# Optimization experiments

Hardware: AMD Instinct MI355X
Metric: run time of the kernel (lower is better)

## Reference

```python
import jax, jax.numpy as jnp
import numpy as np

N = 50000      # nodes
E = 400000     # edges
D = 128        # embedding_depth
H = 4          # attention heads
DK = 32        # per-head dim (graph_message_depth / heads)
NR = 50        # num_radial
L = 2          # num_graph_convolutions
NG = 100       # graphs in batch
NT = 100       # atom type vocab
TE = 32        # atom_type_embedding_dims
OUT = 512      # bottleneck_dim
CUT = 6.0      # convolution_cutoff


def setup_inputs() -> dict:
    key = jax.random.key(0)
    ks = jax.random.split(key, 20)
    s = 0.05
    inp = {
        'pos': jax.random.normal(ks[0], (N, 3), jnp.float32) * 5.0,
        'atom_types': jax.random.randint(ks[1], (N,), 0, NT),
        'edge_index': jax.random.randint(ks[2], (2, E), 0, N),
        'batch': jnp.sort(jax.random.randint(ks[3], (N,), 0, NG)),
        'emb_table': jax.random.normal(ks[4], (NT, TE), jnp.float32) * s,
        'W_init': jax.random.normal(ks[5], (TE + 3, D), jnp.float32) * s,
        'b_init': jnp.zeros((D,), jnp.float32),
        'Wq': jax.random.normal(ks[6], (L, D, H * DK), jnp.float32) * s,
        'Wk': jax.random.normal(ks[7], (L, D, H * DK), jnp.float32) * s,
        'Wv': jax.random.normal(ks[8], (L, D, H * DK), jnp.float32) * s,
        'We': jax.random.normal(ks[9], (L, NR, H * DK), jnp.float32) * s,
        'Wo': jax.random.normal(ks[10], (L, H * DK, D), jnp.float32) * s,
        'Wm1': jax.random.normal(ks[11], (L, D, D), jnp.float32) * s,
        'bm1': jnp.zeros((L, D), jnp.float32),
        'Wm2': jax.random.normal(ks[12], (L, D, D), jnp.float32) * s,
        'bm2': jnp.zeros((L, D), jnp.float32),
        'ln_g': jnp.ones((L, D), jnp.float32),
        'ln_b': jnp.zeros((L, D), jnp.float32),
        'W_out': jax.random.normal(ks[13], (D, OUT), jnp.float32) * s,
        'b_out': jnp.zeros((OUT,), jnp.float32),
    }
    return inp


def _layernorm(x, g, b):
    m = jnp.mean(x, -1, keepdims=True)
    v = jnp.var(x, -1, keepdims=True)
    return (x - m) * jax.lax.rsqrt(v + 1e-5) * g + b


def _rbf(d):
    # Gaussian radial basis with smooth cosine cutoff envelope
    mus = jnp.linspace(0.0, CUT, NR)
    gamma = (NR / CUT) ** 2
    env = 0.5 * (jnp.cos(jnp.pi * jnp.minimum(d, CUT) / CUT) + 1.0)
    return jnp.exp(-gamma * (d[:, None] - mus[None, :]) ** 2) * env[:, None]


def _seg_softmax(logits, seg, n):
    # logits: [E, H], segmented softmax over incoming edges per node
    m = jax.ops.segment_max(logits, seg, num_segments=n)
    e = jnp.exp(logits - m[seg])
    s = jax.ops.segment_sum(e, seg, num_segments=n)
    return e / (s[seg] + 1e-9)


def _forward(pos, atom_types, edge_index, batch, emb_table, W_init, b_init,
             Wq, Wk, Wv, We, Wo, Wm1, bm1, Wm2, bm2, ln_g, ln_b, W_out, b_out):
    src, dst = edge_index[0], edge_index[1]
    # atom type embedding + concat positions -> init node features
    x0 = jnp.concatenate([emb_table[atom_types], pos], axis=-1)  # [N, TE+3]
    x = x0 @ W_init + b_init                                     # [N, D]
    # radial features per edge
    d = jnp.linalg.norm(pos[src] - pos[dst] + 1e-8, axis=-1)     # [E]
    rb = _rbf(d)                                                 # [E, NR]
    scale = 1.0 / jnp.sqrt(jnp.float32(DK))
    for l in range(L):
        qn, kn, vn = x @ Wq[l], x @ Wk[l], x @ Wv[l]             # [N, H*DK]
        q = qn[dst].reshape(E, H, DK)
        k = kn[src].reshape(E, H, DK)
        v = vn[src].reshape(E, H, DK)
        e = (rb @ We[l]).reshape(E, H, DK)
        logits = jnp.sum(q * (k + e), axis=-1) * scale           # [E, H]
        a = _seg_softmax(logits, dst, N)                         # [E, H]
        msg = jax.ops.segment_sum(a[..., None] * (v + e), dst, num_segments=N)
        x = x + msg.reshape(N, H * DK) @ Wo[l]
        # nodewise FC block with pre-norm and residual
        h = _layernorm(x, ln_g[l], ln_b[l])
        h = jax.nn.gelu(h @ Wm1[l] + bm1[l])
        x = x + h @ Wm2[l] + bm2[l]
    # sum graph aggregation, then output projection to bottleneck
    g = jax.ops.segment_sum(x, batch, num_segments=NG)           # [NG, D]
    return g @ W_out + b_out                                     # [NG, OUT]


def reference(pos, atom_types, edge_index, batch, emb_table, W_init, b_init,
              Wq, Wk, Wv, We, Wo, Wm1, bm1, Wm2, bm2, ln_g, ln_b, W_out, b_out):
    return _forward(pos, atom_types, edge_index, batch, emb_table, W_init, b_init,
                    Wq, Wk, Wv, We, Wo, Wm1, bm1, Wm2, bm2, ln_g, ln_b, W_out, b_out)
```

## Files before the change

### kernel.cpp

```cpp
#include <hip/hip_runtime.h>
#include <math.h>

#define NN 50000
#define NE 400000
#define DDIM 128
#define NHEAD 4
#define NRAD 50
#define NGRAPH 100
#define NTYPE 100
#define TEMB 32
#define DOUT 512
#define CUTF 6.0f
#define PI_F 3.14159265358979323846f

#define SCAN_N ((NN + 255) / 256)

typedef unsigned int uint;
typedef unsigned short ushort;
typedef __attribute__((ext_vector_type(8))) short short8;
typedef __attribute__((ext_vector_type(4))) float f32x4;


__device__ __forceinline__ float gelu_tanh(float v) {
  float u = 0.7978845608028654f * (v + 0.044715f * v * v * v);
  return 0.5f * v * (1.0f + tanhf(u));
}

__device__ __forceinline__ ushort f2bf(float f) {
  uint u = __float_as_uint(f);
  uint r = (u + 0x7fffu + ((u >> 16) & 1u)) >> 16;
  return (ushort)r;
}
__device__ __forceinline__ float bfl(uint u) { return __uint_as_float(u << 16); }
__device__ __forceinline__ float bfh(uint u) { return __uint_as_float(u & 0xffff0000u); }

__device__ __forceinline__ float red16(float v) {
  v += __int_as_float(__builtin_amdgcn_update_dpp(0, __float_as_int(v), 0xB1, 0xF, 0xF, true));
  v += __int_as_float(__builtin_amdgcn_update_dpp(0, __float_as_int(v), 0x4E, 0xF, 0xF, true));
  v += __int_as_float(__builtin_amdgcn_update_dpp(0, __float_as_int(v), 0x141, 0xF, 0xF, true));
  v += __int_as_float(__builtin_amdgcn_update_dpp(0, __float_as_int(v), 0x140, 0xF, 0xF, true));
  return v;
}
__device__ __forceinline__ float red8(float v) {
  v += __int_as_float(__builtin_amdgcn_update_dpp(0, __float_as_int(v), 0xB1, 0xF, 0xF, true));
  v += __int_as_float(__builtin_amdgcn_update_dpp(0, __float_as_int(v), 0x4E, 0xF, 0xF, true));
  v += __int_as_float(__builtin_amdgcn_update_dpp(0, __float_as_int(v), 0x141, 0xF, 0xF, true));
  return v;
}

__global__ void k_fill_f(float* p, float v, int n) {
  int i = blockIdx.x * blockDim.x + threadIdx.x;
  if (i < n) p[i] = v;
}
__global__ void k_fill_i(int* p, int v, int n) {
  int i = blockIdx.x * blockDim.x + threadIdx.x;
  if (i < n) p[i] = v;
}


__global__ void k_wconv(const float* __restrict__ Wq, const float* __restrict__ Wk,
                        const float* __restrict__ Wv, const float* __restrict__ Wo,
                        const float* __restrict__ Wm1, const float* __restrict__ Wm2,
                        ushort* __restrict__ Wtb) {
  int idx = blockIdx.x * 256 + threadIdx.x;
  int m = idx >> 14;
  int r = idx & 16383;
  int c = r >> 7, k = r & 127;
  int l = m / 6, fam = m % 6;
  const float* src = fam == 0 ? Wq : fam == 1 ? Wk : fam == 2 ? Wv
                   : fam == 3 ? Wo : fam == 4 ? Wm1 : Wm2;
  Wtb[idx] = f2bf(src[l * 16384 + k * 128 + c]);
}


__global__ void k_wewo(const float* __restrict__ We, const float* __restrict__ Wo,
                       ushort* __restrict__ WW) {
  int idx = blockIdx.x * 256 + threadIdx.x;
  int l = idx >> 15;
  int r = idx & 32767;
  int c = r >> 8, k = r & 255;
  float acc = 0.f;
  if (k < 200) {
    int j = k >> 2, h = k & 3;
    const float* we = We + (size_t)l * NRAD * DDIM + j * DDIM + 32 * h;
    const float* wo = Wo + (size_t)l * DDIM * DDIM + (size_t)(32 * h) * DDIM + c;
#pragma unroll 8
    for (int dk = 0; dk < 32; ++dk) acc = fmaf(we[dk], wo[(size_t)dk * DDIM], acc);
  }
  WW[idx] = f2bf(acc);
}


__global__ void k_embw(const float* __restrict__ emb, const float* __restrict__ W,
                       const float* __restrict__ b, float* __restrict__ embW) {
  int idx = blockIdx.x * 256 + threadIdx.x;
  if (idx >= NTYPE * DDIM) return;
  int a = idx >> 7, c = idx & 127;
  const float* er = emb + (size_t)a * TEMB;
  float acc = b[c];
#pragma unroll
  for (int t = 0; t < TEMB; ++t) acc = fmaf(er[t], W[t * DDIM + c], acc);
  embW[idx] = acc;
}


__global__ void k_init2(const float* __restrict__ pos, const int* __restrict__ at,
                        const float* __restrict__ embW, const float* __restrict__ W,
                        float* __restrict__ x) {
  int idx = blockIdx.x * blockDim.x + threadIdx.x;
  if (idx >= NN * 32) return;
  int n = idx >> 5, c4 = (idx & 31) << 2;
  float4 e = *(const float4*)&embW[(size_t)at[n] * DDIM + c4];
  float px = pos[n * 3 + 0], py = pos[n * 3 + 1], pz = pos[n * 3 + 2];
  float4 wx = *(const float4*)&W[(TEMB + 0) * DDIM + c4];
  float4 wy = *(const float4*)&W[(TEMB + 1) * DDIM + c4];
  float4 wz = *(const float4*)&W[(TEMB + 2) * DDIM + c4];
  float4 o;
  o.x = e.x + px * wx.x + py * wy.x + pz * wz.x;
  o.y = e.y + px * wx.y + py * wy.y + pz * wz.y;
  o.z = e.z + px * wx.z + py * wy.z + pz * wz.z;
  o.w = e.w + px * wx.w + py * wy.w + pz * wz.w;
  *(float4*)&x[(size_t)n * DDIM + c4] = o;
}


__global__ void k_edge(const float* __restrict__ pos, const int* __restrict__ ei,
                       float* __restrict__ de, int* __restrict__ deg) {
  int e = blockIdx.x * blockDim.x + threadIdx.x;
  if (e >= NE) return;
  int s = ei[e], t = ei[NE + e];
  float dx = pos[s * 3 + 0] - pos[t * 3 + 0] + 1e-8f;
  float dy = pos[s * 3 + 1] - pos[t * 3 + 1] + 1e-8f;
  float dz = pos[s * 3 + 2] - pos[t * 3 + 2] + 1e-8f;
  de[e] = sqrtf(dx * dx + dy * dy + dz * dz);
  atomicAdd(&deg[t], 1);
}


__global__ void k_scan1(const int* __restrict__ deg, int* __restrict__ bsum) {
  __shared__ int red[256];
  int i = blockIdx.x * 256 + threadIdx.x;
  red[threadIdx.x] = (i < NN) ? deg[i] : 0;
  __syncthreads();
  for (int off = 128; off > 0; off >>= 1) {
    if (threadIdx.x < off) red[threadIdx.x] += red[threadIdx.x + off];
    __syncthreads();
  }
  if (threadIdx.x == 0) bsum[blockIdx.x] = red[0];
}

__global__ void k_scan2(int* __restrict__ bsum) {
  __shared__ int sh[256];
  int t = threadIdx.x;
  int v = (t < SCAN_N) ? bsum[t] : 0;
  sh[t] = v;
  __syncthreads();
  for (int off = 1; off < 256; off <<= 1) {
    int u = (t >= off) ? sh[t - off] : 0;
    __syncthreads();
    sh[t] += u;
    __syncthreads();
  }
  if (t < SCAN_N) bsum[t] = (t == 0) ? 0 : sh[t - 1];
}

__global__ void k_scan3(const int* __restrict__ deg, const int* __restrict__ bsum,
                        int* __restrict__ rowptr, int* __restrict__ cnear,
                        int* __restrict__ cfar) {
  __shared__ int sh[256];
  int t = threadIdx.x;
  int i = blockIdx.x * 256 + t;
  int v = (i < NN) ? deg[i] : 0;
  sh[t] = v;
  __syncthreads();
  for (int off = 1; off < 256; off <<= 1) {
    int u = (t >= off) ? sh[t - off] : 0;
    __syncthreads();
    sh[t] += u;
    __syncthreads();
  }
  int excl = bsum[blockIdx.x] + sh[t] - v;
  if (i < NN) {
    rowptr[i] = excl;
    cnear[i] = excl;
    cfar[i] = excl + v;
    if (i == NN - 1) rowptr[NN] = excl + v;
  }
}

__global__ void k_scatter(const int* __restrict__ ei, const float* __restrict__ de,
                          int* __restrict__ cnear, int* __restrict__ cfar,
                          int2* __restrict__ er) {
  int e = blockIdx.x * blockDim.x + threadIdx.x;
  if (e >= NE) return;
  int src = ei[e], dst = ei[NE + e];
  float d = de[e];
  int idx;
  if (d < CUTF)
    idx = atomicAdd(&cnear[dst], 1);
  else
    idx = atomicSub(&cfar[dst], 1) - 1;
  er[idx] = make_int2(src, __float_as_int(d));
}


__global__ __launch_bounds__(256) void k_qkv(
    const float* __restrict__ x, const ushort* __restrict__ Wt3,
    ushort* __restrict__ qo, ushort* __restrict__ ko, ushort* __restrict__ vo) {
  __shared__ ushort Al[128 * 128];
  __shared__ ushort Wl[128 * 128];
  const int tid = threadIdx.x;
  const int r0 = blockIdx.x * 128;

  for (int i = tid; i < 128 * 16; i += 256) {
    int r = i >> 4, g = i & 15;
    int gr = r0 + r;
    float4 f0 = {0, 0, 0, 0}, f1 = {0, 0, 0, 0};
    if (gr < NN) {
      f0 = *(const float4*)&x[(size_t)gr * 128 + g * 8];
      f1 = *(const float4*)&x[(size_t)gr * 128 + g * 8 + 4];
    }
    int gs = g ^ (r & 7);
    ushort4 u0 = {f2bf(f0.x), f2bf(f0.y), f2bf(f0.z), f2bf(f0.w)};
    ushort4 u1 = {f2bf(f1.x), f2bf(f1.y), f2bf(f1.z), f2bf(f1.w)};
    *(ushort4*)&Al[r * 128 + gs * 8] = u0;
    *(ushort4*)&Al[r * 128 + gs * 8 + 4] = u1;
  }

  const int w = tid >> 6, l = tid & 63;
  const int lg = l >> 4, lr = l & 15;

  for (int m = 0; m < 3; ++m) {
    for (int i = tid; i < 128 * 16; i += 256) {
      int c = i >> 4, g = i & 15;
      ushort4 w0 = *(const ushort4*)&Wt3[m * 16384 + c * 128 + g * 8];
      ushort4 w1 = *(const ushort4*)&Wt3[m * 16384 + c * 128 + g * 8 + 4];
      int gs = g ^ (c & 7);
      *(ushort4*)&Wl[c * 128 + gs * 8] = w0;
      *(ushort4*)&Wl[c * 128 + gs * 8 + 4] = w1;
    }
    __syncthreads();

    f32x4 acc[2][8];
#pragma unroll
    for (int rt = 0; rt < 2; ++rt)
#pragma unroll
      for (int ct = 0; ct < 8; ++ct) acc[rt][ct] = (f32x4){0.f, 0.f, 0.f, 0.f};

#pragma unroll
    for (int ks = 0; ks < 4; ++ks) {
      short8 af[2];
#pragma unroll
      for (int rt = 0; rt < 2; ++rt) {
        int arow = w * 32 + rt * 16 + lr;
        int ga = (ks * 4 + lg) ^ (arow & 7);
        af[rt] = *(const short8*)&Al[arow * 128 + ga * 8];
      }
#pragma unroll
      for (int ct = 0; ct < 8; ++ct) {
        int col = ct * 16 + lr;
        int gb = (ks * 4 + lg) ^ (col & 7);
        short8 bf = *(const short8*)&Wl[col * 128 + gb * 8];
#pragma unroll
        for (int rt = 0; rt < 2; ++rt)
          acc[rt][ct] = __builtin_amdgcn_mfma_f32_16x16x32_bf16(af[rt], bf, acc[rt][ct], 0, 0, 0);
      }
    }

    ushort* o = (m == 0) ? qo : (m == 1) ? ko : vo;
#pragma unroll
    for (int rt = 0; rt < 2; ++rt)
#pragma unroll
      for (int ct = 0; ct < 8; ++ct) {
        int col = ct * 16 + lr;
#pragma unroll
        for (int r = 0; r < 4; ++r) {
          int row = r0 + w * 32 + rt * 16 + lg * 4 + r;
          if (row < NN) o[(size_t)row * 128 + col] = f2bf(acc[rt][ct][r]);
        }
      }
    __syncthreads();
  }
}


template <bool BIAS, bool GELU, bool RESID, bool LNF, bool EXTK>
__global__ __launch_bounds__(256) void k_gemm2(
    const ushort* __restrict__ A, const ushort* __restrict__ Wt,
    const float* __restrict__ bias, const float* __restrict__ resid,
    void* __restrict__ outp, const float* __restrict__ lng,
    const float* __restrict__ lnb, ushort* __restrict__ lnout,
    const ushort* __restrict__ arbn, const ushort* __restrict__ WW) {
  __shared__ ushort Al[128 * 128];
  __shared__ ushort Wl[128 * 128];
  const int tid = threadIdx.x;
  const int r0 = blockIdx.x * 128;

  for (int i = tid; i < 128 * 16; i += 256) {
    int r = i >> 4, g = i & 15;
    int gr = r0 + r;
    ushort4 v0 = {0, 0, 0, 0}, v1 = {0, 0, 0, 0};
    if (gr < NN) {
      v0 = *(const ushort4*)&A[(size_t)gr * 128 + g * 8];
      v1 = *(const ushort4*)&A[(size_t)gr * 128 + g * 8 + 4];
    }
    int gs = g ^ (r & 7);
    *(ushort4*)&Al[r * 128 + gs * 8] = v0;
    *(ushort4*)&Al[r * 128 + gs * 8 + 4] = v1;
  }
  for (int i = tid; i < 128 * 16; i += 256) {
    int c = i >> 4, g = i & 15;
    ushort4 w0 = *(const ushort4*)&Wt[c * 128 + g * 8];
    ushort4 w1 = *(const ushort4*)&Wt[c * 128 + g * 8 + 4];
    int gs = g ^ (c & 7);
    *(ushort4*)&Wl[c * 128 + gs * 8] = w0;
    *(ushort4*)&Wl[c * 128 + gs * 8 + 4] = w1;
  }
  __syncthreads();

  const int w = tid >> 6, l = tid & 63;
  const int lg = l >> 4, lr = l & 15;
  f32x4 acc[2][8];
#pragma unroll
  for (int rt = 0; rt < 2; ++rt)
#pragma unroll
    for (int ct = 0; ct < 8; ++ct) acc[rt][ct] = (f32x4){0.f, 0.f, 0.f, 0.f};

#pragma unroll
  for (int ks = 0; ks < 4; ++ks) {
    short8 af[2];
#pragma unroll
    for (int rt = 0; rt < 2; ++rt) {
      int arow = w * 32 + rt * 16 + lr;
      int ga = (ks * 4 + lg) ^ (arow & 7);
      af[rt] = *(const short8*)&Al[arow * 128 + ga * 8];
    }
#pragma unroll
    for (int ct = 0; ct < 8; ++ct) {
      int col = ct * 16 + lr;
      int gb = (ks * 4 + lg) ^ (col & 7);
      short8 bf = *(const short8*)&Wl[col * 128 + gb * 8];
#pragma unroll
      for (int rt = 0; rt < 2; ++rt)
        acc[rt][ct] = __builtin_amdgcn_mfma_f32_16x16x32_bf16(af[rt], bf, acc[rt][ct], 0, 0, 0);
    }
  }

  if (EXTK) {
    for (int q = 0; q < 2; ++q) {
      __syncthreads();
      for (int i = tid; i < 128 * 16; i += 256) {
        int r = i >> 4, g = i & 15;
        int gr = r0 + r;
        ushort4 v0 = {0, 0, 0, 0}, v1 = {0, 0, 0, 0};
        if (gr < NN && (q == 0 || g < 9)) {
          v0 = *(const ushort4*)&arbn[(size_t)gr * 200 + q * 128 + g * 8];
          v1 = *(const ushort4*)&arbn[(size_t)gr * 200 + q * 128 + g * 8 + 4];
        }
        int gs = g ^ (r & 7);
        *(ushort4*)&Al[r * 128 + gs * 8] = v0;
        *(ushort4*)&Al[r * 128 + gs * 8 + 4] = v1;
      }
      for (int i = tid; i < 128 * 16; i += 256) {
        int c = i >> 4, g = i & 15;
        ushort4 w0 = *(const ushort4*)&WW[c * 256 + q * 128 + g * 8];
        ushort4 w1 = *(const ushort4*)&WW[c * 256 + q * 128 + g * 8 + 4];
        int gs = g ^ (c & 7);
        *(ushort4*)&Wl[c * 128 + gs * 8] = w0;
        *(ushort4*)&Wl[c * 128 + gs * 8 + 4] = w1;
      }
      __syncthreads();
#pragma unroll
      for (int ks = 0; ks < 4; ++ks) {
        short8 af[2];
#pragma unroll
        for (int rt = 0; rt < 2; ++rt) {
          int arow = w * 32 + rt * 16 + lr;
          int ga = (ks * 4 + lg) ^ (arow & 7);
          af[rt] = *(const short8*)&Al[arow * 128 + ga * 8];
        }
#pragma unroll
        for (int ct = 0; ct < 8; ++ct) {
          int col = ct * 16 + lr;
          int gb = (ks * 4 + lg) ^ (col & 7);
          short8 bf = *(const short8*)&Wl[col * 128 + gb * 8];
#pragma unroll
          for (int rt = 0; rt < 2; ++rt)
            acc[rt][ct] = __builtin_amdgcn_mfma_f32_16x16x32_bf16(af[rt], bf, acc[rt][ct], 0, 0, 0);
        }
      }
    }
  }

#pragma unroll
  for (int rt = 0; rt < 2; ++rt)
#pragma unroll
    for (int r = 0; r < 4; ++r) {
      int row = r0 + w * 32 + rt * 16 + lg * 4 + r;
      bool ok = row < NN;
      float v[8];
#pragma unroll
      for (int ct = 0; ct < 8; ++ct) {
        int col = ct * 16 + lr;
        float vv = acc[rt][ct][r];
        if (BIAS) vv += bias[col];
        if (GELU) vv = gelu_tanh(vv);
        if (RESID) vv += ok ? resid[(size_t)row * 128 + col] : 0.f;
        v[ct] = vv;
      }
      if (RESID || LNF) {
        if (ok)
#pragma unroll
          for (int ct = 0; ct < 8; ++ct)
            ((float*)outp)[(size_t)row * 128 + ct * 16 + lr] = v[ct];
      } else {
        if (ok)
#pragma unroll
          for (int ct = 0; ct < 8; ++ct)
            ((ushort*)outp)[(size_t)row * 128 + ct * 16 + lr] = f2bf(v[ct]);
      }
      if (LNF) {
        float s = 0.f, ss = 0.f;
#pragma unroll
        for (int ct = 0; ct < 8; ++ct) {
          s += v[ct];
          ss = fmaf(v[ct], v[ct], ss);
        }
#pragma unroll
        for (int msk = 8; msk >= 1; msk >>= 1) {
          s += __shfl_xor(s, msk);
          ss += __shfl_xor(ss, msk);
        }
        float mean = s * (1.0f / DDIM);
        float var = ss * (1.0f / DDIM) - mean * mean;
        float inv = rsqrtf(var + 1e-5f);
        if (ok)
#pragma unroll
          for (int ct = 0; ct < 8; ++ct) {
            int col = ct * 16 + lr;
            lnout[(size_t)row * 128 + col] =
                f2bf((v[ct] - mean) * inv * lng[col] + lnb[col]);
          }
      }
    }
}


__global__ __launch_bounds__(256) void k_qe(const ushort* __restrict__ qnb,
                                            const float* __restrict__ We,
                                            ushort* __restrict__ qe) {
  __shared__ float Wlds[NRAD][DDIM + 1];
  __shared__ float qlds[4][DDIM];
  int tid = threadIdx.x;
  for (int i = tid; i < NRAD * DDIM; i += 256) Wlds[i / DDIM][i % DDIM] = We[i];
  __syncthreads();
  int w = tid >> 6, t = tid & 63;
  for (int rep = 0; rep < 2; ++rep) {
    int n = blockIdx.x * 8 + rep * 4 + w;
    uint qu = *(const uint*)&qnb[(size_t)n * DDIM + 2 * t];
    qlds[w][2 * t] = bfl(qu);
    qlds[w][2 * t + 1] = bfh(qu);
    if (t < NRAD) {
      float e0 = 0.f, e1 = 0.f, e2 = 0.f, e3 = 0.f;
#pragma unroll
      for (int d = 0; d < 32; ++d) e0 = fmaf(Wlds[t][d], qlds[w][d], e0);
#pragma unroll
      for (int d = 32; d < 64; ++d) e1 = fmaf(Wlds[t][d], qlds[w][d], e1);
#pragma unroll
      for (int d = 64; d < 96; ++d) e2 = fmaf(Wlds[t][d], qlds[w][d], e2);
#pragma unroll
      for (int d = 96; d < 128; ++d) e3 = fmaf(Wlds[t][d], qlds[w][d], e3);
      ushort4 o = {f2bf(e0), f2bf(e1), f2bf(e2), f2bf(e3)};
      *(ushort4*)&qe[(size_t)n * 200 + 4 * t] = o;
    }
  }
}


__device__ __forceinline__ float rbf_fill(float d, int j) {
  const float step = CUTF / (NRAD - 1);
  const float gamma = (NRAD / CUTF) * (NRAD / CUTF);
  float mu = j * step;
  float dm = d - mu;
  float env = 0.5f * (__cosf(PI_F * d / CUTF) + 1.0f);
  return __expf(-gamma * dm * dm) * env;
}

#define SCALE_QK 0.17677669529663687f

__global__ __launch_bounds__(256) void k_attn7(
    const ushort* __restrict__ qnb, const ushort* __restrict__ knb,
    const ushort* __restrict__ vnb, ushort* __restrict__ qe,
    const int2* __restrict__ er, const int* __restrict__ rowptr,
    const int* __restrict__ nearend, ushort* __restrict__ msgb) {
  __shared__ float qel[4][64][4];
  __shared__ float rbl[4][64];
  __shared__ float aml[4][128];
  const int tid = threadIdx.x;

  const int w = tid >> 6, t = tid & 63;
  const int n = blockIdx.x * 4 + w;
  const int h = t >> 4;
  const int j0 = t & 15;
  const int hw = t >> 5;
  const int c = t & 31;
  uint qu = *(const uint*)&qnb[(size_t)n * DDIM + 2 * t];
  const float q0 = bfl(qu), q1 = bfh(qu);
  uint2 qp = *(const uint2*)&qnb[(size_t)n * DDIM + 4 * c];
  const float fq0 = bfl(qp.x), fq1 = bfh(qp.x), fq2 = bfl(qp.y), fq3 = bfh(qp.y);
  if (t < NRAD) {
    ushort4 qv = *(const ushort4*)&qe[(size_t)n * 200 + 4 * t];
    qel[w][t][0] = bfl(qv.x);
    qel[w][t][1] = bfl(qv.y);
    qel[w][t][2] = bfl(qv.z);
    qel[w][t][3] = bfl(qv.w);
  } else {
    qel[w][t][0] = 0.f; qel[w][t][1] = 0.f; qel[w][t][2] = 0.f; qel[w][t][3] = 0.f;
  }
  const int start = rowptr[n], nend = nearend[n], end = rowptr[n + 1];

  float s = 0.f, a0 = 0.f, a1 = 0.f;
  float4 arb = {0.f, 0.f, 0.f, 0.f};

  for (int cb = start; cb < nend; cb += 64) {
    int cnt = min(nend - cb, 64);
    int2 e_t = make_int2(0, 0);
    if (t < cnt) e_t = er[cb + t];
    for (int i = 0; i < cnt; ++i) {
      int src = __shfl(e_t.x, i);
      float dd = __shfl(__int_as_float(e_t.y), i);
      uint ku = *(const uint*)&knb[(size_t)src * DDIM + 2 * t];
      uint vu = *(const uint*)&vnb[(size_t)src * DDIM + 2 * t];
      float pr = q0 * bfl(ku) + q1 * bfh(ku);
      float rb = (t < NRAD) ? rbf_fill(dd, t) : 0.f;
      rbl[w][t] = rb;
      pr = fmaf(rbl[w][j0], qel[w][j0][h], pr);
      pr = fmaf(rbl[w][j0 + 16], qel[w][j0 + 16][h], pr);
      pr = fmaf(rbl[w][j0 + 32], qel[w][j0 + 32][h], pr);
      pr = fmaf(rbl[w][j0 + 48], qel[w][j0 + 48][h], pr);
      pr = red16(pr);
      float ae = __expf(fminf(pr * SCALE_QK, 60.f));
      s += ae;
      a0 = fmaf(ae, bfl(vu), a0);
      a1 = fmaf(ae, bfh(vu), a1);
      float aex = __shfl(ae, 0);
      float aey = __shfl(ae, 16);
      float aez = __shfl(ae, 32);
      float aew = __shfl(ae, 48);
      arb.x = fmaf(rb, aex, arb.x);
      arb.y = fmaf(rb, aey, arb.y);
      arb.z = fmaf(rb, aez, arb.z);
      arb.w = fmaf(rb, aew, arb.w);
    }
  }

  float sf = 0.f, af0 = 0.f, af1 = 0.f, af2 = 0.f, af3 = 0.f;
  for (int cb = nend; cb < end; cb += 64) {
    int cnt = min(end - cb, 64);
    int src_t = 0;
    if (t < cnt) src_t = er[cb + t].x;
    for (int i = hw; i < cnt; i += 2) {
      int src = __shfl(src_t, i);
      uint2 ku = *(const uint2*)&knb[(size_t)src * DDIM + 4 * c];
      uint2 vu = *(const uint2*)&vnb[(size_t)src * DDIM + 4 * c];
      float pr = fq0 * bfl(ku.x) + fq1 * bfh(ku.x);
      pr = fmaf(fq2, bfl(ku.y), pr);
      pr = fmaf(fq3, bfh(ku.y), pr);
      pr = red8(pr);
      float ae = __expf(fminf(pr * SCALE_QK, 60.f));
      sf += ae;
      af0 = fmaf(ae, bfl(vu.x), af0);
      af1 = fmaf(ae, bfh(vu.x), af1);
      af2 = fmaf(ae, bfl(vu.y), af2);
      af3 = fmaf(ae, bfh(vu.y), af3);
    }
  }
  sf += __shfl_xor(sf, 32);
  af0 += __shfl_xor(af0, 32);
  af1 += __shfl_xor(af1, 32);
  af2 += __shfl_xor(af2, 32);
  af3 += __shfl_xor(af3, 32);
  aml[w][4 * c + 0] = af0;
  aml[w][4 * c + 1] = af1;
  aml[w][4 * c + 2] = af2;
  aml[w][4 * c + 3] = af3;
  a0 += aml[w][2 * t];
  a1 += aml[w][2 * t + 1];

  float4 s4;
  s4.x = __shfl(s, 0) + __shfl(sf, 0);
  s4.y = __shfl(s, 16) + __shfl(sf, 8);
  s4.z = __shfl(s, 32) + __shfl(sf, 16);
  s4.w = __shfl(s, 48) + __shfl(sf, 24);
  float4 inv4 = {1.f / (s4.x + 1e-9f), 1.f / (s4.y + 1e-9f),
                 1.f / (s4.z + 1e-9f), 1.f / (s4.w + 1e-9f)};
  float invo = (h == 0) ? inv4.x : (h == 1) ? inv4.y : (h == 2) ? inv4.z : inv4.w;
  if (t < NRAD) {
    ushort4 o = {f2bf(arb.x * inv4.x), f2bf(arb.y * inv4.y),
                 f2bf(arb.z * inv4.z), f2bf(arb.w * inv4.w)};
    *(ushort4*)&qe[(size_t)n * 200 + 4 * t] = o;
  }
  a0 *= invo;
  a1 *= invo;
  uint pk = (uint)f2bf(a0) | ((uint)f2bf(a1) << 16);
  *(uint*)&msgb[(size_t)n * DDIM + 2 * t] = pk;
}


#define GS_NODES 32
__global__ void k_graphsum(const float* __restrict__ x, const int* __restrict__ batch,
                           float* __restrict__ g) {
  int t = threadIdx.x;
  int n0 = blockIdx.x * GS_NODES;
  int nend = n0 + GS_NODES;
  if (nend > NN) nend = NN;
  if (n0 >= NN) return;
  float acc = 0.f;
  int cur = batch[n0];
  for (int n = n0; n < nend; ++n) {
    int bb = batch[n];
    if (bb != cur) {
      atomicAdd(&g[(size_t)cur * DDIM + t], acc);
      acc = 0.f;
      cur = bb;
    }
    acc += x[(size_t)n * DDIM + t];
  }
  atomicAdd(&g[(size_t)cur * DDIM + t], acc);
}


__global__ void k_out(const float* __restrict__ g, const float* __restrict__ W,
                      const float* __restrict__ b, float* __restrict__ out) {
  int idx = blockIdx.x * blockDim.x + threadIdx.x;
  if (idx >= NGRAPH * DOUT) return;
  int r = idx / DOUT, c = idx % DOUT;
  float acc = b[c];
#pragma unroll 8
  for (int k = 0; k < DDIM; ++k) acc = fmaf(g[r * DDIM + k], W[k * DOUT + c], acc);
  out[idx] = acc;
}


extern "C" void kernel_launch(void* const* d_in, const int* in_sizes, int n_in,
                              void* d_out, int out_size, void* d_ws, size_t ws_size,
                              hipStream_t stream) {
  const float* pos = (const float*)d_in[0];
  const int* at = (const int*)d_in[1];
  const int* ei = (const int*)d_in[2];
  const int* batch = (const int*)d_in[3];
  const float* emb = (const float*)d_in[4];
  const float* W_init = (const float*)d_in[5];
  const float* b_init = (const float*)d_in[6];
  const float* Wq = (const float*)d_in[7];
  const float* Wk = (const float*)d_in[8];
  const float* Wv = (const float*)d_in[9];
  const float* We = (const float*)d_in[10];
  const float* Wo = (const float*)d_in[11];
  const float* Wm1 = (const float*)d_in[12];
  const float* bm1 = (const float*)d_in[13];
  const float* Wm2 = (const float*)d_in[14];
  const float* bm2 = (const float*)d_in[15];
  const float* ln_g = (const float*)d_in[16];
  const float* ln_b = (const float*)d_in[17];
  const float* W_out = (const float*)d_in[18];
  const float* b_out = (const float*)d_in[19];
  float* out = (float*)d_out;

  const size_t ND = (size_t)NN * DDIM;
  float* x = (float*)d_ws;
  ushort* qnb = (ushort*)(x + ND);
  ushort* knb = qnb + ND;
  ushort* vnb = knb + ND;
  ushort* msgb = vnb + ND;
  ushort* qe = msgb + ND;
  ushort* Wtb = qe + (size_t)NN * 200;
  ushort* WW = Wtb + 12 * 16384;
  float* embW = (float*)(WW + 2 * 32768);
  float* de = embW + NTYPE * DDIM;
  int* deg = (int*)(de + NE);
  int* cnear = deg + NN;
  int* cfar = cnear + NN;
  int* rowptr = cfar + NN;
  int2* er = (int2*)(rowptr + NN + 64);
  float* gb = (float*)(er + NE);
  int* bsum = (int*)(gb + NGRAPH * DDIM);

  ushort* hb = qnb;
  ushort* h2 = knb;

  k_wconv<<<12 * 16384 / 256, 256, 0, stream>>>(Wq, Wk, Wv, Wo, Wm1, Wm2, Wtb);
  k_wewo<<<2 * 32768 / 256, 256, 0, stream>>>(We, Wo, WW);
  k_embw<<<(NTYPE * DDIM + 255) / 256, 256, 0, stream>>>(emb, W_init, b_init, embW);
  k_fill_i<<<(NN + 255) / 256, 256, 0, stream>>>(deg, 0, NN);
  k_init2<<<(NN * 32 + 255) / 256, 256, 0, stream>>>(pos, at, embW, W_init, x);
  k_edge<<<(NE + 255) / 256, 256, 0, stream>>>(pos, ei, de, deg);
  k_scan1<<<SCAN_N, 256, 0, stream>>>(deg, bsum);
  k_scan2<<<1, 256, 0, stream>>>(bsum);
  k_scan3<<<SCAN_N, 256, 0, stream>>>(deg, bsum, rowptr, cnear, cfar);
  k_scatter<<<(NE + 255) / 256, 256, 0, stream>>>(ei, de, cnear, cfar, er);

  const int gg = (NN + 127) / 128;
  for (int l = 0; l < 2; ++l) {
    const ushort* Wt_l = Wtb + (size_t)l * 6 * 16384;
    const float* We_l = We + (size_t)l * NRAD * DDIM;
    const ushort* WW_l = WW + (size_t)l * 32768;

    k_qkv<<<gg, 256, 0, stream>>>(x, Wt_l, qnb, knb, vnb);
    k_qe<<<NN / 8, 256, 0, stream>>>(qnb, We_l, qe);
    k_attn7<<<NN / 4, 256, 0, stream>>>(qnb, knb, vnb, qe, er, rowptr, cnear, msgb);

    k_gemm2<false, false, true, true, true><<<gg, 256, 0, stream>>>(
        msgb, Wt_l + 3 * 16384, nullptr, x, x,
        ln_g + (size_t)l * DDIM, ln_b + (size_t)l * DDIM, hb, qe, WW_l);
    k_gemm2<true, true, false, false, false><<<gg, 256, 0, stream>>>(
        hb, Wt_l + 4 * 16384, bm1 + (size_t)l * DDIM, nullptr, h2,
        nullptr, nullptr, nullptr, nullptr, nullptr);
    k_gemm2<true, false, true, false, false><<<gg, 256, 0, stream>>>(
        h2, Wt_l + 5 * 16384, bm2 + (size_t)l * DDIM, x, x,
        nullptr, nullptr, nullptr, nullptr, nullptr);
  }

  k_fill_f<<<(NGRAPH * DDIM + 255) / 256, 256, 0, stream>>>(gb, 0.f, NGRAPH * DDIM);
  k_graphsum<<<(NN + GS_NODES - 1) / GS_NODES, 128, 0, stream>>>(x, batch, gb);
  k_out<<<(NGRAPH * DOUT + 255) / 256, 256, 0, stream>>>(gb, W_out, b_out, out);
}
```

Measured before the change: 431.2 us.

## Fold q·We projection into QKV GEMM via precomputed Wq·We weights

Precomputes a combined Wq×We^T weight matrix (200 columns padded to 256, bf16) once per layer. The QKV MFMA kernel then runs two extra column passes to produce the per-node q·e table directly from x. This removes the separate k_qe kernel, along with its re-read of q and its scalar FMA loops. In exchange, k_qkv does more MFMA work and adds output passes, and q·e now comes from bf16 x and fused weights rather than rounded q, which changes the rounding.

Result: faster. 357.3 us (-17.1%).

```diff
diff --git a/kernel.cpp b/kernel.cpp
--- a/kernel.cpp
+++ b/kernel.cpp
@@ -88,6 +88,24 @@
     for (int dk = 0; dk < 32; ++dk) acc = fmaf(we[dk], wo[(size_t)dk * DDIM], acc);
   }
   WW[idx] = f2bf(acc);
+}
+
+
+__global__ void k_wqe(const float* __restrict__ Wq, const float* __restrict__ We,
+                      ushort* __restrict__ WQET) {
+  int idx = blockIdx.x * 256 + threadIdx.x;
+  int l = idx >> 15;
+  int r = idx & 32767;
+  int col = r >> 7, d = r & 127;
+  float acc = 0.f;
+  if (col < 200) {
+    int j = col >> 2, h = col & 3;
+    const float* wq = Wq + (size_t)l * 16384 + (size_t)d * 128 + 32 * h;
+    const float* we = We + (size_t)l * NRAD * DDIM + j * DDIM + 32 * h;
+#pragma unroll 8
+    for (int u = 0; u < 32; ++u) acc = fmaf(wq[u], we[u], acc);
+  }
+  WQET[idx] = f2bf(acc);
 }
 
 
@@ -206,7 +224,8 @@
 
 __global__ __launch_bounds__(256) void k_qkv(
     const float* __restrict__ x, const ushort* __restrict__ Wt3,
-    ushort* __restrict__ qo, ushort* __restrict__ ko, ushort* __restrict__ vo) {
+    const ushort* __restrict__ WQET, ushort* __restrict__ qo,
+    ushort* __restrict__ ko, ushort* __restrict__ vo, ushort* __restrict__ qe) {
   __shared__ ushort Al[128 * 128];
   __shared__ ushort Wl[128 * 128];
   const int tid = threadIdx.x;
@@ -230,11 +249,12 @@
   const int w = tid >> 6, l = tid & 63;
   const int lg = l >> 4, lr = l & 15;
 
-  for (int m = 0; m < 3; ++m) {
+  for (int m = 0; m < 5; ++m) {
+    const ushort* wsrc = (m < 3) ? (Wt3 + m * 16384) : (WQET + (m - 3) * 16384);
     for (int i = tid; i < 128 * 16; i += 256) {
       int c = i >> 4, g = i & 15;
-      ushort4 w0 = *(const ushort4*)&Wt3[m * 16384 + c * 128 + g * 8];
-      ushort4 w1 = *(const ushort4*)&Wt3[m * 16384 + c * 128 + g * 8 + 4];
+      ushort4 w0 = *(const ushort4*)&wsrc[c * 128 + g * 8];
+      ushort4 w1 = *(const ushort4*)&wsrc[c * 128 + g * 8 + 4];
       int gs = g ^ (c & 7);
       *(ushort4*)&Wl[c * 128 + gs * 8] = w0;
       *(ushort4*)&Wl[c * 128 + gs * 8 + 4] = w1;
@@ -267,18 +287,35 @@
       }
     }
 
-    ushort* o = (m == 0) ? qo : (m == 1) ? ko : vo;
-#pragma unroll
-    for (int rt = 0; rt < 2; ++rt)
-#pragma unroll
-      for (int ct = 0; ct < 8; ++ct) {
-        int col = ct * 16 + lr;
-#pragma unroll
-        for (int r = 0; r < 4; ++r) {
-          int row = r0 + w * 32 + rt * 16 + lg * 4 + r;
-          if (row < NN) o[(size_t)row * 128 + col] = f2bf(acc[rt][ct][r]);
+    if (m < 3) {
+      ushort* o = (m == 0) ? qo : (m == 1) ? ko : vo;
+#pragma unroll
+      for (int rt = 0; rt < 2; ++rt)
+#pragma unroll
+        for (int ct = 0; ct < 8; ++ct) {
+          int col = ct * 16 + lr;
+#pragma unroll
+          for (int r = 0; r < 4; ++r) {
+            int row = r0 + w * 32 + rt * 16 + lg * 4 + r;
+            if (row < NN) o[(size_t)row * 128 + col] = f2bf(acc[rt][ct][r]);
+          }
         }
-      }
+    } else {
+      int cb = (m - 3) * 128;
+#pragma unroll
+      for (int rt = 0; rt < 2; ++rt)
+#pragma unroll
+        for (int ct = 0; ct < 8; ++ct) {
+          int col = cb + ct * 16 + lr;
+          if (col < 200) {
+#pragma unroll
+            for (int r = 0; r < 4; ++r) {
+              int row = r0 + w * 32 + rt * 16 + lg * 4 + r;
+              if (row < NN) qe[(size_t)row * 200 + col] = f2bf(acc[rt][ct][r]);
+            }
+          }
+        }
+    }
     __syncthreads();
   }
 }
@@ -443,37 +480,6 @@
           }
       }
     }
-}
-
-
-__global__ __launch_bounds__(256) void k_qe(const ushort* __restrict__ qnb,
-                                            const float* __restrict__ We,
-                                            ushort* __restrict__ qe) {
-  __shared__ float Wlds[NRAD][DDIM + 1];
-  __shared__ float qlds[4][DDIM];
-  int tid = threadIdx.x;
-  for (int i = tid; i < NRAD * DDIM; i += 256) Wlds[i / DDIM][i % DDIM] = We[i];
-  __syncthreads();
-  int w = tid >> 6, t = tid & 63;
-  for (int rep = 0; rep < 2; ++rep) {
-    int n = blockIdx.x * 8 + rep * 4 + w;
-    uint qu = *(const uint*)&qnb[(size_t)n * DDIM + 2 * t];
-    qlds[w][2 * t] = bfl(qu);
-    qlds[w][2 * t + 1] = bfh(qu);
-    if (t < NRAD) {
-      float e0 = 0.f, e1 = 0.f, e2 = 0.f, e3 = 0.f;
-#pragma unroll
-      for (int d = 0; d < 32; ++d) e0 = fmaf(Wlds[t][d], qlds[w][d], e0);
-#pragma unroll
-      for (int d = 32; d < 64; ++d) e1 = fmaf(Wlds[t][d], qlds[w][d], e1);
-#pragma unroll
-      for (int d = 64; d < 96; ++d) e2 = fmaf(Wlds[t][d], qlds[w][d], e2);
-#pragma unroll
-      for (int d = 96; d < 128; ++d) e3 = fmaf(Wlds[t][d], qlds[w][d], e3);
-      ushort4 o = {f2bf(e0), f2bf(e1), f2bf(e2), f2bf(e3)};
-      *(ushort4*)&qe[(size_t)n * 200 + 4 * t] = o;
-    }
-  }
 }
 
 
@@ -676,7 +682,8 @@
   ushort* qe = msgb + ND;
   ushort* Wtb = qe + (size_t)NN * 200;
   ushort* WW = Wtb + 12 * 16384;
-  float* embW = (float*)(WW + 2 * 32768);
+  ushort* WQET = WW + 2 * 32768;
+  float* embW = (float*)(WQET + 2 * 32768);
   float* de = embW + NTYPE * DDIM;
   int* deg = (int*)(de + NE);
   int* cnear = deg + NN;
@@ -691,6 +698,7 @@
 
   k_wconv<<<12 * 16384 / 256, 256, 0, stream>>>(Wq, Wk, Wv, Wo, Wm1, Wm2, Wtb);
   k_wewo<<<2 * 32768 / 256, 256, 0, stream>>>(We, Wo, WW);
+  k_wqe<<<2 * 32768 / 256, 256, 0, stream>>>(Wq, We, WQET);
   k_embw<<<(NTYPE * DDIM + 255) / 256, 256, 0, stream>>>(emb, W_init, b_init, embW);
   k_fill_i<<<(NN + 255) / 256, 256, 0, stream>>>(deg, 0, NN);
   k_init2<<<(NN * 32 + 255) / 256, 256, 0, stream>>>(pos, at, embW, W_init, x);
@@ -703,11 +711,10 @@
   const int gg = (NN + 127) / 128;
   for (int l = 0; l < 2; ++l) {
     const ushort* Wt_l = Wtb + (size_t)l * 6 * 16384;
-    const float* We_l = We + (size_t)l * NRAD * DDIM;
+    const ushort* WQET_l = WQET + (size_t)l * 32768;
     const ushort* WW_l = WW + (size_t)l * 32768;
 
-    k_qkv<<<gg, 256, 0, stream>>>(x, Wt_l, qnb, knb, vnb);
-    k_qe<<<NN / 8, 256, 0, stream>>>(qnb, We_l, qe);
+    k_qkv<<<gg, 256, 0, stream>>>(x, Wt_l, WQET_l, qnb, knb, vnb, qe);
     k_attn7<<<NN / 4, 256, 0, stream>>>(qnb, knb, vnb, qe, er, rowptr, cnear, msgb);
 
     k_gemm2<false, false, true, true, true><<<gg, 256, 0, stream>>>(
```
